# Optimization experiments

Hardware: AMD Instinct MI355X
Metric: run time of the kernel (lower is better)

The kernel has to match this reference:

```python
import jax, jax.numpy as jnp
import numpy as np

N = 50000      # nodes
E = 800000     # edges
F = 128        # node_features
DSS = 64       # degree_set_size
H = 128        # latent dim (hardcoded in GraphES)


def gcn_conv(x, W, b, src, dst, n):
    # PyG GCNConv: linear -> symmetric-normalized aggregation with self loops -> bias
    h = x @ W                                            # [N, C_out]
    deg = jnp.zeros((n,), x.dtype).at[dst].add(1.0) + 1.0  # in-degree incl. self loop
    dinv = jax.lax.rsqrt(deg)
    norm = dinv[src] * dinv[dst]                         # [E]
    agg = jnp.zeros_like(h).at[dst].add(h[src] * norm[:, None])
    agg = agg + h * (dinv * dinv)[:, None]               # self-loop term (norm_ii = 1/deg_i)
    return agg + b


def mlp(x, w1, b1, w2, b2):
    return jax.nn.relu(x @ w1 + b1) @ w2 + b2


def _swap(ei, i1, i2, coin):
    e1 = jnp.take(ei, i1, axis=1)
    e2 = jnp.take(ei, i2, axis=1)
    a, b = e1[0], e1[1]
    c, d = e2[0], e2[1]
    ne1 = jnp.where(coin, jnp.stack([a, d]), jnp.stack([a, c]))
    ne2 = jnp.where(coin, jnp.stack([c, b]), jnp.stack([b, d]))
    return ei.at[:, i1].set(ne1).at[:, i2].set(ne2)


def setup_inputs() -> dict:
    key = jax.random.key(0)
    ks = jax.random.split(key, 24)
    s = 0.05

    def rn(k, shape):
        return jax.random.normal(k, shape, jnp.float32) * s

    return {
        "x": jax.random.normal(ks[0], (N, F), jnp.float32),
        "edge_index": jax.random.randint(ks[1], (2, E), 0, N, dtype=jnp.int32),
        "degree_set": jax.random.randint(ks[2], (N,), 0, DSS, dtype=jnp.int32),
        "timesteps": 5,
        # encoder: GCN(F+DSS -> 2H), GCN(2H -> H)
        "enc_w1": rn(ks[3], (F + DSS, 2 * H)), "enc_b1": jnp.zeros((2 * H,), jnp.float32),
        "enc_w2": rn(ks[4], (2 * H, H)),       "enc_b2": jnp.zeros((H,), jnp.float32),
        # decoder: GCN(H+DSS -> 2F), GCN(2F -> F)
        "dec_w1": rn(ks[5], (H + DSS, 2 * F)), "dec_b1": jnp.zeros((2 * F,), jnp.float32),
        "dec_w2": rn(ks[6], (2 * F, F)),       "dec_b2": jnp.zeros((F,), jnp.float32),
        # edge_predictor_1: Linear(128,64)->ReLU->Linear(64,1)
        "ep1_w1": rn(ks[7], (H, 64)),  "ep1_b1": jnp.zeros((64,), jnp.float32),
        "ep1_w2": rn(ks[8], (64, 1)),  "ep1_b2": jnp.zeros((1,), jnp.float32),
        # edge_predictor_2: input is z concat flattened pair features -> 128+256=384
        "ep2_w1": rn(ks[9], (H + 2 * H, 64)), "ep2_b1": jnp.zeros((64,), jnp.float32),
        "ep2_w2": rn(ks[10], (64, 1)),        "ep2_b2": jnp.zeros((1,), jnp.float32),
    }


def reference(x, edge_index, degree_set, timesteps,
              enc_w1, enc_b1, enc_w2, enc_b2,
              dec_w1, dec_b1, dec_w2, dec_b2,
              ep1_w1, ep1_b1, ep1_w2, ep1_b2,
              ep2_w1, ep2_b1, ep2_w2, ep2_b2):
    src, dst = edge_index[0], edge_index[1]
    dh = jax.nn.one_hot(degree_set, DSS, dtype=x.dtype)  # [N, DSS]

    # ---- encoder ----
    h = jax.nn.relu(gcn_conv(jnp.concatenate([x, dh], 1), enc_w1, enc_b1, src, dst, N))
    z = gcn_conv(h, enc_w2, enc_b2, src, dst, N)          # [N, H]

    # ---- forward diffusion: timesteps random edge swaps (deterministic PRNG) ----
    ei = edge_index
    for t in range(timesteps):
        k1, k2 = jax.random.split(jax.random.fold_in(jax.random.key(1), t))
        idx = jax.random.choice(k1, E, (2,), replace=False)
        ei = _swap(ei, idx[0], idx[1], jax.random.bernoulli(k2))

    # ---- reverse process: argmax-driven edge swaps ----
    # edge_predictor_1 scores depend only on z -> identical every step; compute once
    i1 = jnp.argmax(mlp(z, ep1_w1, ep1_b1, ep1_w2, ep1_b2).squeeze(-1))
    for t in range(timesteps):
        e1 = jnp.take(ei, i1, axis=1)                     # [2]
        e1f = z[e1].reshape(-1)                           # [2H]
        cond = jnp.concatenate([z, jnp.broadcast_to(e1f, (N, 2 * H))], 1)
        i2 = jnp.argmax(mlp(cond, ep2_w1, ep2_b1, ep2_w2, ep2_b2).squeeze(-1))
        coin = jax.random.bernoulli(jax.random.fold_in(jax.random.key(2), t))
        ei = _swap(ei, i1, i2, coin)

    # ---- decoder on final edge structure ----
    src2, dst2 = ei[0], ei[1]
    hd = jax.nn.relu(gcn_conv(jnp.concatenate([z, dh], 1), dec_w1, dec_b1, src2, dst2, N))
    out = gcn_conv(hd, dec_w2, dec_b2, src2, dst2, N)     # [N, F]
    return out, ei
```

## Files before the change

kernel.cpp:

```cpp
#include <hip/hip_runtime.h>
#include <cstdint>
#include <cstddef>
#include <vector>
#include <algorithm>

#define NN 50000
#define EE 800000
#define FF 128
#define HH 128
#define TSTEPS 5

typedef __attribute__((ext_vector_type(8))) short bf16x8;
typedef __attribute__((ext_vector_type(4))) float f32x4;

__device__ __forceinline__ float bf2f(unsigned short u)
{
    return __uint_as_float((unsigned)u << 16);
}
__device__ __forceinline__ unsigned short f2bf(float x)
{
    unsigned u = __float_as_uint(x);
    u = (u + 0x7FFFu + ((u >> 16) & 1u));
    return (unsigned short)(u >> 16);
}
__device__ __forceinline__ void splitbf(float v, unsigned short& hi, unsigned short& lo)
{
    hi = f2bf(v);
    lo = f2bf(v - bf2f(hi));
}

__device__ __forceinline__ void gload16(const void* g, void* l)
{
    __builtin_amdgcn_global_load_lds(
        (const __attribute__((address_space(1))) void*)g,
        (__attribute__((address_space(3))) void*)l, 16, 0, 0);
}

__global__ __launch_bounds__(256, 4) void zw1_gemm(
    const float* __restrict__ A, const float* __restrict__ Wp4,
    float* __restrict__ Pout, int n, const float* __restrict__ bias)
{
    __shared__ float As[32][128];
    const int row0 = blockIdx.x * 32;
    const int tid = threadIdx.x;
    for (int idx = tid; idx < 32 * 32; idx += 256) {
        int r = idx >> 5, k4 = idx & 31;
        int gr = row0 + r;
        float4 v = make_float4(0.f, 0.f, 0.f, 0.f);
        if (gr < n) v = ((const float4*)(A + (size_t)gr * 128))[k4];
        *(float4*)&As[r][k4 * 4] = v;
    }
    __syncthreads();
    const int w = tid >> 6, l = tid & 63;
    float acc[8];
#pragma unroll
    for (int r = 0; r < 8; r++) acc[r] = 0.f;

#pragma unroll 2
    for (int k4 = 0; k4 < 32; k4++) {
        float4 wv = ((const float4*)Wp4)[k4 * 64 + l];
#pragma unroll
        for (int r = 0; r < 8; r++) {
            float4 zv = *(const float4*)&As[w * 8 + r][k4 * 4];
            acc[r] = fmaf(zv.x, wv.x, acc[r]);
            acc[r] = fmaf(zv.y, wv.y, acc[r]);
            acc[r] = fmaf(zv.z, wv.z, acc[r]);
            acc[r] = fmaf(zv.w, wv.w, acc[r]);
        }
    }
    float bv = bias[l];
#pragma unroll
    for (int r = 0; r < 8; r++) {
        int gr = row0 + w * 8 + r;
        if (gr < n) Pout[(size_t)gr * 64 + l] = acc[r] + bv;
    }
}

template <int K, int C, int BC, int WR, int WC, bool HAS_BIAS, bool RELU>
__global__ __launch_bounds__(256) void gemm_bf16_tiled(
    const unsigned short* __restrict__ A, const unsigned short* __restrict__ Wp,
    unsigned short* __restrict__ Pout, const float* __restrict__ bias, int n)
{
    constexpr int KC = K / 32;
    constexpr int RT = 128 / (WR * 16);
    constexpr int TT = BC / (WC * 16);
    constexpr int STAGE_USHORTS = 4096 + BC * 32;
    constexpr int OT_USHORTS = 128 * BC;
    constexpr int LDS_USHORTS = (STAGE_USHORTS > OT_USHORTS) ? STAGE_USHORTS : OT_USHORTS;
    __shared__ __align__(16) unsigned short smem[LDS_USHORTS];
    unsigned short* AL = smem;
    unsigned short* WL = smem + 4096;

    const int row0 = blockIdx.x * 128;
    const int col0 = blockIdx.y * BC;
    const int tid = threadIdx.x;
    const int w = tid >> 6, l = tid & 63;
    const int m = l & 15, quad = l >> 4;
    const int wr = w / WC, wc = w % WC;
    const int rowBase = wr * (RT * 16);
    const int colBase = wc * (TT * 16);

    f32x4 acc[RT][TT];
#pragma unroll
    for (int rt = 0; rt < RT; rt++)
#pragma unroll
        for (int tt = 0; tt < TT; tt++) acc[rt][tt] = { 0.f, 0.f, 0.f, 0.f };

    for (int kc = 0; kc < KC; kc++) {
        for (int s = w; s < 8; s += 4) {
            int rg = row0 + s * 16 + (l >> 2);
            if (rg > n - 1) rg = n - 1;
            size_t go = (size_t)rg * K + kc * 32 + (l & 3) * 8;
            gload16(A + go, AL + s * 512);
        }
        for (int s = w; s < BC / 16; s += 4) {
            size_t wo = ((size_t)kc * C + col0) * 32 + s * 512 + l * 8;
            gload16(Wp + wo, WL + s * 512);
        }
        __syncthreads();

        bf16x8 a[RT];
#pragma unroll
        for (int rt = 0; rt < RT; rt++)
            a[rt] = *(const bf16x8*)(AL + (rowBase + rt * 16 + m) * 32 + quad * 8);
#pragma unroll
        for (int tt = 0; tt < TT; tt++) {
            bf16x8 b = *(const bf16x8*)(WL + (colBase + tt * 16 + m) * 32 + quad * 8);
#pragma unroll
            for (int rt = 0; rt < RT; rt++)
                acc[rt][tt] = __builtin_amdgcn_mfma_f32_16x16x32_bf16(a[rt], b, acc[rt][tt], 0, 0, 0);
        }
        __syncthreads();
    }

    unsigned short* Ot = smem;
#pragma unroll
    for (int tt = 0; tt < TT; tt++) {
        int col_in = colBase + tt * 16 + m;
        float bv = HAS_BIAS ? bias[col0 + col_in] : 0.f;
#pragma unroll
        for (int rt = 0; rt < RT; rt++)
#pragma unroll
            for (int r = 0; r < 4; r++) {
                int row_in = rowBase + rt * 16 + quad * 4 + r;
                float v = acc[rt][tt][r] + bv;
                if (RELU) v = fmaxf(v, 0.f);
                Ot[row_in * BC + col_in] = f2bf(v);
            }
    }
    __syncthreads();
    for (int idx = tid; idx < 128 * (BC / 8); idx += 256) {
        int rr = idx / (BC / 8), c8 = idx - rr * (BC / 8);
        int gr = row0 + rr;
        if (gr < n)
            *(bf16x8*)(Pout + (size_t)gr * C + col0 + c8 * 8) =
                *(const bf16x8*)(Ot + rr * BC + c8 * 8);
    }
}

template <int K, int C, int BC, int WR, int WC, bool HAS_BIAS, bool RELU, bool OUT_SPLIT>
__global__ __launch_bounds__(256) void gemm_split_tiled(
    const unsigned short* __restrict__ Ahi, const unsigned short* __restrict__ Alo,
    const unsigned short* __restrict__ Whi, const unsigned short* __restrict__ Wlo,
    void* __restrict__ PoutHi, unsigned short* __restrict__ PoutLo,
    const float* __restrict__ bias, int n)
{
    constexpr int KC = K / 32;
    constexpr int RT = 128 / (WR * 16);
    constexpr int TT = BC / (WC * 16);
    constexpr int LDS_USHORTS = 8192 + BC * 64;
    __shared__ __align__(16) unsigned short smem[LDS_USHORTS];
    unsigned short* AhL = smem;
    unsigned short* AlL = smem + 4096;
    unsigned short* WhL = smem + 8192;
    unsigned short* WlL = smem + 8192 + BC * 32;

    const int row0 = blockIdx.x * 128;
    const int col0 = blockIdx.y * BC;
    const int tid = threadIdx.x;
    const int w = tid >> 6, l = tid & 63;
    const int m = l & 15, quad = l >> 4;
    const int wr = w / WC, wc = w % WC;
    const int rowBase = wr * (RT * 16);
    const int colBase = wc * (TT * 16);

    f32x4 acc[RT][TT];
#pragma unroll
    for (int rt = 0; rt < RT; rt++)
#pragma unroll
        for (int tt = 0; tt < TT; tt++) acc[rt][tt] = { 0.f, 0.f, 0.f, 0.f };

    for (int kc = 0; kc < KC; kc++) {
        for (int s = w; s < 8; s += 4) {
            int rg = row0 + s * 16 + (l >> 2);
            if (rg > n - 1) rg = n - 1;
            size_t go = (size_t)rg * K + kc * 32 + (l & 3) * 8;
            gload16(Ahi + go, AhL + s * 512);
            gload16(Alo + go, AlL + s * 512);
        }
        for (int s = w; s < BC / 16; s += 4) {
            size_t wo = ((size_t)kc * C + col0) * 32 + s * 512 + l * 8;
            gload16(Whi + wo, WhL + s * 512);
            gload16(Wlo + wo, WlL + s * 512);
        }
        __syncthreads();

        bf16x8 ah[RT], al[RT];
#pragma unroll
        for (int rt = 0; rt < RT; rt++) {
            int ro = (rowBase + rt * 16 + m) * 32 + quad * 8;
            ah[rt] = *(const bf16x8*)(AhL + ro);
            al[rt] = *(const bf16x8*)(AlL + ro);
        }
#pragma unroll
        for (int tt = 0; tt < TT; tt++) {
            int co = (colBase + tt * 16 + m) * 32 + quad * 8;
            bf16x8 wh = *(const bf16x8*)(WhL + co);
            bf16x8 wl = *(const bf16x8*)(WlL + co);
#pragma unroll
            for (int rt = 0; rt < RT; rt++) {
                acc[rt][tt] = __builtin_amdgcn_mfma_f32_16x16x32_bf16(al[rt], wh, acc[rt][tt], 0, 0, 0);
                acc[rt][tt] = __builtin_amdgcn_mfma_f32_16x16x32_bf16(ah[rt], wl, acc[rt][tt], 0, 0, 0);
                acc[rt][tt] = __builtin_amdgcn_mfma_f32_16x16x32_bf16(ah[rt], wh, acc[rt][tt], 0, 0, 0);
            }
        }
        __syncthreads();
    }

    if (OUT_SPLIT) {
        unsigned short* Ot = smem;
#pragma unroll
        for (int tt = 0; tt < TT; tt++) {
            int col_in = colBase + tt * 16 + m;
            float bv = HAS_BIAS ? bias[col0 + col_in] : 0.f;
#pragma unroll
            for (int rt = 0; rt < RT; rt++)
#pragma unroll
                for (int r = 0; r < 4; r++) {
                    int row_in = rowBase + rt * 16 + quad * 4 + r;
                    float v = acc[rt][tt][r] + bv;
                    if (RELU) v = fmaxf(v, 0.f);
                    Ot[row_in * BC + col_in] = f2bf(v);
                }
        }
        __syncthreads();
        for (int idx = tid; idx < 128 * (BC / 8); idx += 256) {
            int rr = idx / (BC / 8), c8 = idx - rr * (BC / 8);
            int gr = row0 + rr;
            if (gr < n)
                *(bf16x8*)((unsigned short*)PoutHi + (size_t)gr * C + col0 + c8 * 8) =
                    *(const bf16x8*)(Ot + rr * BC + c8 * 8);
        }
        __syncthreads();
#pragma unroll
        for (int tt = 0; tt < TT; tt++) {
            int col_in = colBase + tt * 16 + m;
            float bv = HAS_BIAS ? bias[col0 + col_in] : 0.f;
#pragma unroll
            for (int rt = 0; rt < RT; rt++)
#pragma unroll
                for (int r = 0; r < 4; r++) {
                    int row_in = rowBase + rt * 16 + quad * 4 + r;
                    float v = acc[rt][tt][r] + bv;
                    if (RELU) v = fmaxf(v, 0.f);
                    unsigned short h = f2bf(v);
                    Ot[row_in * BC + col_in] = f2bf(v - bf2f(h));
                }
        }
        __syncthreads();
        for (int idx = tid; idx < 128 * (BC / 8); idx += 256) {
            int rr = idx / (BC / 8), c8 = idx - rr * (BC / 8);
            int gr = row0 + rr;
            if (gr < n)
                *(bf16x8*)(PoutLo + (size_t)gr * C + col0 + c8 * 8) =
                    *(const bf16x8*)(Ot + rr * BC + c8 * 8);
        }
    } else {
#pragma unroll
        for (int tt = 0; tt < TT; tt++) {
            int col = col0 + colBase + tt * 16 + m;
            float bv = HAS_BIAS ? bias[col] : 0.f;
#pragma unroll
            for (int rt = 0; rt < RT; rt++)
#pragma unroll
                for (int r = 0; r < 4; r++) {
                    int gr = row0 + rowBase + rt * 16 + quad * 4 + r;
                    if (gr >= n) continue;
                    float v = acc[rt][tt][r] + bv;
                    if (RELU) v = fmaxf(v, 0.f);
                    ((float*)PoutHi)[(size_t)gr * C + col] = v;
                }
        }
    }
}

template <int K, int C>
__global__ void pack_w(const float* __restrict__ W, unsigned short* __restrict__ Wp)
{
    int idx = blockIdx.x * 256 + threadIdx.x;
    if (idx >= K * C) return;
    int k = idx / C, nn = idx - k * C;
    Wp[((size_t)(k >> 5) * C + nn) * 32 + (k & 31)] = f2bf(W[idx]);
}

template <int K, int C>
__global__ void pack_w_split(const float* __restrict__ W,
                             unsigned short* __restrict__ Wphi,
                             unsigned short* __restrict__ Wplo)
{
    int idx = blockIdx.x * 256 + threadIdx.x;
    if (idx >= K * C) return;
    int k = idx / C, nn = idx - k * C;
    unsigned short hi, lo;
    splitbf(W[idx], hi, lo);
    size_t o = ((size_t)(k >> 5) * C + nn) * 32 + (k & 31);
    Wphi[o] = hi;
    Wplo[o] = lo;
}

template <int K, int C>
__global__ void pack_w4(const float* __restrict__ W, float* __restrict__ Wp4)
{
    int idx = blockIdx.x * 256 + threadIdx.x;
    if (idx >= K * C) return;
    int k = idx / C, c = idx - k * C;
    Wp4[(((size_t)(k >> 2) * C) + c) * 4 + (k & 3)] = W[idx];
}

__global__ void count_deg(const int* __restrict__ dst, int* __restrict__ cnt, int e)
{
    int i = blockIdx.x * blockDim.x + threadIdx.x;
    if (i < e) {
        unsigned d = (unsigned)dst[i];
        if (d < (unsigned)NN) atomicAdd(&cnt[d], 1);
    }
}

__global__ void scan_block(const int* __restrict__ cnt, int* __restrict__ excl,
                           int* __restrict__ bsum, float* __restrict__ dinv, int n)
{
    __shared__ int s[256];
    int i = blockIdx.x * 256 + threadIdx.x;
    int v = (i < n) ? cnt[i] : 0;
    if (i < n) dinv[i] = 1.0f / sqrtf((float)v + 1.0f);
    s[threadIdx.x] = v;
    __syncthreads();
    for (int off = 1; off < 256; off <<= 1) {
        int t = (threadIdx.x >= off) ? s[threadIdx.x - off] : 0;
        __syncthreads();
        s[threadIdx.x] += t;
        __syncthreads();
    }
    if (i < n) excl[i] = s[threadIdx.x] - v;
    if (threadIdx.x == 255) bsum[blockIdx.x] = s[255];
}
__global__ void scan_add_fill(int* __restrict__ rowptr, const int* __restrict__ bsum,
                              int* __restrict__ fill, int n, int e)
{
    int pre = 0;
    for (int b = 0; b < (int)blockIdx.x; b++) pre += bsum[b];
    int i = blockIdx.x * 256 + threadIdx.x;
    if (i < n) { rowptr[i] += pre; fill[i] = 0; }
    if (i == 0) rowptr[n] = e;
}

__global__ void csr_fill_pairs(const int* __restrict__ src, const int* __restrict__ dst,
                               const float* __restrict__ dinv, const int* __restrict__ rowptr,
                               int* __restrict__ fill, int* __restrict__ csr_src,
                               float* __restrict__ csr_nrm, int e)
{
    int i = blockIdx.x * blockDim.x + threadIdx.x;
    if (i >= e) return;
    int d = dst[i], s = src[i];
    if ((unsigned)d >= (unsigned)NN || (unsigned)s >= (unsigned)NN) return;
    int slot = rowptr[d] + atomicAdd(&fill[d], 1);
    csr_src[slot] = s;
    csr_nrm[slot] = dinv[s] * dinv[d];
}

template <bool BF16SRC, int OUTMODE>
__global__ __launch_bounds__(256) void agg_feat(
    const void* __restrict__ Xv, const int* __restrict__ ds,
    const int* __restrict__ rowptr, const int* __restrict__ csr_src,
    const float* __restrict__ csr_nrm, const float* __restrict__ dinv,
    void* __restrict__ Fout, unsigned short* __restrict__ FoutLo)
{
    const int w = threadIdx.x >> 6, l = threadIdx.x & 63;
    const int i = blockIdx.x * 4 + w;
    if (i >= NN) return;
    const int half = l >> 5, lh = l & 31;

    auto loadRow4 = [&](int s, float* v) {
        if (BF16SRC) {
            ushort4 u = ((const ushort4*)((const unsigned short*)Xv + (size_t)s * 128))[lh];
            v[0] = bf2f(u.x); v[1] = bf2f(u.y); v[2] = bf2f(u.z); v[3] = bf2f(u.w);
        } else {
            float4 t = ((const float4*)((const float*)Xv + (size_t)s * 128))[lh];
            v[0] = t.x; v[1] = t.y; v[2] = t.z; v[3] = t.w;
        }
    };

    float di = dinv[i], d2 = di * di;
    float acc[4];
    {
        float sv[4];
        loadRow4(i, sv);
        float wgt = half ? 0.f : d2;
#pragma unroll
        for (int v = 0; v < 4; v++) acc[v] = sv[v] * wgt;
    }
    float hist = (ds[i] == l) ? d2 : 0.f;

    const int beg = rowptr[i], end = rowptr[i + 1];
    int idx = beg;
    for (; idx + 8 <= end; idx += 8) {
        int s[8]; float nw[8]; int b[8];
#pragma unroll
        for (int j = 0; j < 8; j++) { s[j] = csr_src[idx + j]; nw[j] = csr_nrm[idx + j]; }
#pragma unroll
        for (int j = 0; j < 8; j++) b[j] = ds[s[j]];
        float vv[4][4];
#pragma unroll
        for (int p = 0; p < 4; p++) loadRow4(s[2 * p + half], vv[p]);
#pragma unroll
        for (int p = 0; p < 4; p++) {
            float wp = nw[2 * p + half];
#pragma unroll
            for (int v = 0; v < 4; v++) acc[v] = fmaf(vv[p][v], wp, acc[v]);
        }
#pragma unroll
        for (int j = 0; j < 8; j++) hist += (b[j] == l) ? nw[j] : 0.f;
    }
    for (; idx + 2 <= end; idx += 2) {
        int s0 = csr_src[idx], s1 = csr_src[idx + 1];
        float n0 = csr_nrm[idx], n1 = csr_nrm[idx + 1];
        int b0 = ds[s0], b1 = ds[s1];
        float v0[4];
        loadRow4(half ? s1 : s0, v0);
        float wp = half ? n1 : n0;
#pragma unroll
        for (int v = 0; v < 4; v++) acc[v] = fmaf(v0[v], wp, acc[v]);
        hist += (b0 == l) ? n0 : 0.f;
        hist += (b1 == l) ? n1 : 0.f;
    }
    if (idx < end) {
        int s0 = csr_src[idx];
        float n0 = csr_nrm[idx];
        int b0 = ds[s0];
        float v0[4];
        loadRow4(s0, v0);
        float wp = half ? 0.f : n0;
#pragma unroll
        for (int v = 0; v < 4; v++) acc[v] = fmaf(v0[v], wp, acc[v]);
        hist += (b0 == l) ? n0 : 0.f;
    }
#pragma unroll
    for (int v = 0; v < 4; v++) acc[v] += __shfl_xor(acc[v], 32, 64);

    if (OUTMODE == 2) {
        if (half == 0) {
            unsigned short h[4], lo[4];
#pragma unroll
            for (int v = 0; v < 4; v++) splitbf(acc[v], h[v], lo[v]);
            ((ushort4*)((unsigned short*)Fout + (size_t)i * 192))[lh] =
                make_ushort4(h[0], h[1], h[2], h[3]);
            ((ushort4*)(FoutLo + (size_t)i * 192))[lh] =
                make_ushort4(lo[0], lo[1], lo[2], lo[3]);
        }
        unsigned short hh, ll;
        splitbf(hist, hh, ll);
        ((unsigned short*)Fout)[(size_t)i * 192 + 128 + l] = hh;
        FoutLo[(size_t)i * 192 + 128 + l] = ll;
    } else if (OUTMODE == 1) {
        if (half == 0) {
            ((ushort4*)((unsigned short*)Fout + (size_t)i * 192))[lh] =
                make_ushort4(f2bf(acc[0]), f2bf(acc[1]), f2bf(acc[2]), f2bf(acc[3]));
        }
        ((unsigned short*)Fout)[(size_t)i * 192 + 128 + l] = f2bf(hist);
    } else {
        if (half == 0) {
            ((float4*)((float*)Fout + (size_t)i * 192))[lh] =
                make_float4(acc[0], acc[1], acc[2], acc[3]);
        }
        ((float*)Fout)[(size_t)i * 192 + 128 + l] = hist;
    }
}

template <bool RELU, bool BF16P>
__global__ __launch_bounds__(256) void agg_wave(
    const void* __restrict__ Pv, const int* __restrict__ rowptr,
    const int* __restrict__ csr_src, const float* __restrict__ csr_nrm,
    const float* __restrict__ dinv, const float* __restrict__ bias,
    float* __restrict__ B, unsigned short* __restrict__ Bbf)
{
    const int w = threadIdx.x >> 6, l = threadIdx.x & 63;
    const int i = blockIdx.x * 4 + w;
    if (i >= NN) return;
    const int half = l >> 5, lh = l & 31;

    auto loadRow4 = [&](int s, float* v) {
        if (BF16P) {
            ushort4 u = ((const ushort4*)((const unsigned short*)Pv + (size_t)s * 128))[lh];
            v[0] = bf2f(u.x); v[1] = bf2f(u.y); v[2] = bf2f(u.z); v[3] = bf2f(u.w);
        } else {
            float4 t = ((const float4*)((const float*)Pv + (size_t)s * 128))[lh];
            v[0] = t.x; v[1] = t.y; v[2] = t.z; v[3] = t.w;
        }
    };

    float di = dinv[i], d2 = di * di;
    float acc[4];
    {
        float sv[4];
        loadRow4(i, sv);
        float wgt = half ? 0.f : d2;
#pragma unroll
        for (int v = 0; v < 4; v++) acc[v] = sv[v] * wgt;
    }

    const int beg = rowptr[i], end = rowptr[i + 1];
    int idx = beg;
    for (; idx + 8 <= end; idx += 8) {
        int s[8]; float nw[8];
#pragma unroll
        for (int j = 0; j < 8; j++) { s[j] = csr_src[idx + j]; nw[j] = csr_nrm[idx + j]; }
        float vv[4][4];
#pragma unroll
        for (int p = 0; p < 4; p++) loadRow4(s[2 * p + half], vv[p]);
#pragma unroll
        for (int p = 0; p < 4; p++) {
            float wp = nw[2 * p + half];
#pragma unroll
            for (int v = 0; v < 4; v++) acc[v] = fmaf(vv[p][v], wp, acc[v]);
        }
    }
    for (; idx + 2 <= end; idx += 2) {
        int s0 = csr_src[idx], s1 = csr_src[idx + 1];
        float n0 = csr_nrm[idx], n1 = csr_nrm[idx + 1];
        float v0[4];
        loadRow4(half ? s1 : s0, v0);
        float wp = half ? n1 : n0;
#pragma unroll
        for (int v = 0; v < 4; v++) acc[v] = fmaf(v0[v], wp, acc[v]);
    }
    if (idx < end) {
        int s0 = csr_src[idx];
        float n0 = csr_nrm[idx];
        float v0[4];
        loadRow4(s0, v0);
        float wp = half ? 0.f : n0;
#pragma unroll
        for (int v = 0; v < 4; v++) acc[v] = fmaf(v0[v], wp, acc[v]);
    }
#pragma unroll
    for (int v = 0; v < 4; v++) acc[v] += __shfl_xor(acc[v], 32, 64);

    if (half == 0) {
        float r[4];
#pragma unroll
        for (int v = 0; v < 4; v++) {
            r[v] = acc[v] + bias[lh * 4 + v];
            if (RELU) r[v] = fmaxf(r[v], 0.f);
        }
        ((float4*)(B + (size_t)i * 128))[lh] = make_float4(r[0], r[1], r[2], r[3]);
        if (Bbf)
            ((ushort4*)(Bbf + (size_t)i * 128))[lh] =
                make_ushort4(f2bf(r[0]), f2bf(r[1]), f2bf(r[2]), f2bf(r[3]));
    }
}

__device__ __forceinline__ unsigned long long packScore(float s, int i)
{
    unsigned u = __float_as_uint(s);
    u = (u & 0x80000000u) ? ~u : (u | 0x80000000u);
    return ((unsigned long long)u << 32) | (unsigned)(~(unsigned)i);
}
__device__ __forceinline__ int unpackIdx(unsigned long long v)
{
    return (int)(~(unsigned)(v & 0xFFFFFFFFull));
}
__device__ __forceinline__ unsigned long long maxu64(unsigned long long a,
                                                     unsigned long long b)
{
    return a > b ? a : b;
}

__device__ __forceinline__ void publishBest(
    unsigned long long* blockBest, unsigned* counter, unsigned long long bv,
    int nblocks, unsigned* isLastFlag)
{
    __hip_atomic_store(&blockBest[blockIdx.x], bv, __ATOMIC_RELEASE,
                       __HIP_MEMORY_SCOPE_AGENT);
    unsigned prev = __hip_atomic_fetch_add(counter, 1u, __ATOMIC_ACQ_REL,
                                           __HIP_MEMORY_SCOPE_AGENT);
    *isLastFlag = (prev == (unsigned)(nblocks - 1)) ? 1u : 0u;
}
__device__ __forceinline__ unsigned long long loadBest(
    const unsigned long long* blockBest, int i)
{
    return __hip_atomic_load(&blockBest[i], __ATOMIC_RELAXED,
                             __HIP_MEMORY_SCOPE_AGENT);
}

__global__ __launch_bounds__(256, 4) void score1_blocks(
    const float* __restrict__ z, const float* __restrict__ w1p4,
    const float* __restrict__ b1, const float* __restrict__ w2,
    unsigned long long* __restrict__ blockBest,
    unsigned long long* __restrict__ out, unsigned* __restrict__ counter,
    int n, int nblocks)
{
    __shared__ float Zs[64][HH];
    __shared__ unsigned long long red[4];
    __shared__ unsigned isLast;
    const int row0 = blockIdx.x * 64;
    const int tid = threadIdx.x;
    for (int idx = tid; idx < 64 * 32; idx += 256) {
        int r = idx >> 5, k4 = idx & 31;
        int gr = row0 + r;
        float4 v = make_float4(0.f, 0.f, 0.f, 0.f);
        if (gr < n) v = ((const float4*)(z + (size_t)gr * HH))[k4];
        *(float4*)&Zs[r][k4 * 4] = v;
    }
    __syncthreads();

    const int w = tid >> 6, l = tid & 63;
    float b1v = b1[l], w2v = w2[l];
    unsigned long long best = 0;
    for (int rg = 0; rg < 4; rg++) {
        const int rbase = w * 16 + rg * 4;
        float acc[4];
#pragma unroll
        for (int r = 0; r < 4; r++) acc[r] = b1v;
#pragma unroll 4
        for (int k4 = 0; k4 < 32; k4++) {
            float4 wv = ((const float4*)w1p4)[k4 * 64 + l];
#pragma unroll
            for (int r = 0; r < 4; r++) {
                float4 zv = *(const float4*)&Zs[rbase + r][k4 * 4];
                acc[r] = fmaf(zv.x, wv.x, acc[r]);
                acc[r] = fmaf(zv.y, wv.y, acc[r]);
                acc[r] = fmaf(zv.z, wv.z, acc[r]);
                acc[r] = fmaf(zv.w, wv.w, acc[r]);
            }
        }
#pragma unroll
        for (int r = 0; r < 4; r++) {
            float p = fmaxf(acc[r], 0.f) * w2v;
#pragma unroll
            for (int off = 32; off > 0; off >>= 1) p += __shfl_xor(p, off, 64);
            int row = row0 + rbase + r;
            if (row < n) best = maxu64(best, packScore(p, row));
        }
    }
    if (l == 0) red[w] = best;
    __syncthreads();
    if (tid == 0) {
        unsigned long long bv = maxu64(maxu64(red[0], red[1]), maxu64(red[2], red[3]));
        publishBest(blockBest, counter, bv, nblocks, &isLast);
    }
    __syncthreads();
    if (isLast) {
        unsigned long long b = 0;
        for (int i = tid; i < nblocks; i += 256) b = maxu64(b, loadBest(blockBest, i));
#pragma unroll
        for (int off = 32; off > 0; off >>= 1)
            b = maxu64(b, (unsigned long long)__shfl_xor((long long)b, off, 64));
        if ((tid & 63) == 0) red[tid >> 6] = b;
        __syncthreads();
        if (tid == 0) {
            *out = maxu64(maxu64(red[0], red[1]), maxu64(red[2], red[3]));
            __hip_atomic_store(counter, 0u, __ATOMIC_RELAXED, __HIP_MEMORY_SCOPE_AGENT);
        }
    }
}

__global__ __launch_bounds__(256) void score2_fused(
    int* __restrict__ ei, const unsigned long long* __restrict__ best1,
    const float* __restrict__ z, const float* __restrict__ w1,
    const float* __restrict__ zw1, const float* __restrict__ w2,
    unsigned long long* __restrict__ blockBest, unsigned* __restrict__ counter,
    int n, int coin)
{
    __shared__ float za_s[HH], zb_s[HH];
    __shared__ float cpart[4][64];
    __shared__ float Cs[64], W2s[64];
    __shared__ unsigned long long red[4];
    __shared__ unsigned isLast;
    int i1 = unpackIdx(*best1);
    if ((unsigned)i1 >= (unsigned)EE) i1 = 0;
    int a = ei[i1], b = ei[EE + i1];
    if ((unsigned)a >= (unsigned)NN) a = 0;
    if ((unsigned)b >= (unsigned)NN) b = 0;
    const int tid = threadIdx.x;
    if (tid < HH) za_s[tid] = z[(size_t)a * HH + tid];
    else          zb_s[tid - HH] = z[(size_t)b * HH + tid - HH];
    __syncthreads();
    const int h = tid & 63, kg = tid >> 6;
    float accc = 0.f;
#pragma unroll
    for (int kk = 0; kk < 32; kk++) {
        int k = kg * 32 + kk;
        accc = fmaf(za_s[k], w1[(128 + k) * 64 + h], accc);
        accc = fmaf(zb_s[k], w1[(256 + k) * 64 + h], accc);
    }
    cpart[kg][h] = accc;
    __syncthreads();
    if (tid < 64) {
        Cs[tid] = (cpart[0][tid] + cpart[1][tid]) + (cpart[2][tid] + cpart[3][tid]);
        W2s[tid] = w2[tid];
    }
    __syncthreads();
    const int w = kg, l = h;
    unsigned long long best = 0;
    for (int i = blockIdx.x * 4 + w; i < n; i += gridDim.x * 4) {
        float v = zw1[(size_t)i * 64 + l] + Cs[l];
        v = fmaxf(v, 0.f) * W2s[l];
#pragma unroll
        for (int off = 32; off > 0; off >>= 1) v += __shfl_xor(v, off, 64);
        best = maxu64(best, packScore(v, i));
    }
    if (l == 0) red[w] = best;
    __syncthreads();
    const int nblocks = (int)gridDim.x;
    if (tid == 0) {
        unsigned long long bv = maxu64(maxu64(red[0], red[1]), maxu64(red[2], red[3]));
        publishBest(blockBest, counter, bv, nblocks, &isLast);
    }
    __syncthreads();
    if (isLast) {
        unsigned long long bb = 0;
        for (int i = tid; i < nblocks; i += 256) bb = maxu64(bb, loadBest(blockBest, i));
#pragma unroll
        for (int off = 32; off > 0; off >>= 1)
            bb = maxu64(bb, (unsigned long long)__shfl_xor((long long)bb, off, 64));
        if ((tid & 63) == 0) red[tid >> 6] = bb;
        __syncthreads();
        if (tid == 0) {
            unsigned long long bestv = maxu64(maxu64(red[0], red[1]), maxu64(red[2], red[3]));
            int i2 = unpackIdx(bestv);
            if ((unsigned)i2 >= (unsigned)EE) i2 = 0;
            int A = ei[i1], B = ei[EE + i1], C = ei[i2], D = ei[EE + i2];
            ei[i1] = A;             ei[EE + i1] = coin ? D : C;
            ei[i2] = coin ? C : B;  ei[EE + i2] = coin ? B : D;
            __hip_atomic_store(counter, 0u, __ATOMIC_RELAXED, __HIP_MEMORY_SCOPE_AGENT);
        }
    }
}

struct Swaps { int a[TSTEPS]; int b[TSTEPS]; unsigned coins; };

__global__ void fwd_swaps_k(int* __restrict__ ei, Swaps s)
{
    if (threadIdx.x != 0 || blockIdx.x != 0) return;
    for (int t = 0; t < TSTEPS; t++) {
        int i1 = s.a[t], i2 = s.b[t];
        if ((unsigned)i1 >= (unsigned)EE || (unsigned)i2 >= (unsigned)EE) continue;
        int coin = (s.coins >> t) & 1;
        int A = ei[i1], B = ei[EE + i1], C = ei[i2], D = ei[EE + i2];
        ei[i1] = A;             ei[EE + i1] = coin ? D : C;
        ei[i2] = coin ? C : B;  ei[EE + i2] = coin ? B : D;
    }
}

__global__ void write_out(const float* __restrict__ outF, const int* __restrict__ ei,
                          float* __restrict__ dst)
{
    int i = blockIdx.x * 256 + threadIdx.x;
    if (i < NN * FF) {
        float v = outF[i];
        v = fminf(fmaxf(v, -64.f), 64.f);
        dst[i] = v;
    } else if (i < NN * FF + 2 * EE) {
        dst[i] = (float)ei[i - NN * FF];
    }
}

static inline uint32_t rotl32(uint32_t x, int n) { return (x << n) | (x >> (32 - n)); }

static void tf(uint32_t k0, uint32_t k1, uint32_t c0, uint32_t c1,
               uint32_t& o0, uint32_t& o1)
{
    uint32_t ks[3] = { k0, k1, k0 ^ k1 ^ 0x1BD11BDAu };
    uint32_t x0 = c0 + ks[0], x1 = c1 + ks[1];
    static const int rA[4] = { 13, 15, 26, 6 };
    static const int rB[4] = { 17, 29, 16, 24 };
    for (int g = 0; g < 5; g++) {
        const int* r = (g & 1) ? rB : rA;
        for (int j = 0; j < 4; j++) { x0 += x1; x1 = rotl32(x1, r[j]); x1 ^= x0; }
        x0 += ks[(g + 1) % 3];
        x1 += ks[(g + 2) % 3] + (uint32_t)(g + 1);
    }
    o0 = x0; o1 = x1;
}

static void jsplit_part(uint32_t k0, uint32_t k1,
                        uint32_t& a0, uint32_t& a1, uint32_t& b0, uint32_t& b1)
{
    tf(k0, k1, 0u, 0u, a0, a1);
    tf(k0, k1, 0u, 1u, b0, b1);
}

static void jbits_part(uint32_t k0, uint32_t k1, uint32_t n, std::vector<uint32_t>& out)
{
    out.resize(n);
    for (uint32_t i = 0; i < n; i++) {
        uint32_t a, b;
        tf(k0, k1, 0u, i, a, b);
        out[i] = a ^ b;
    }
}

static bool jbern_part(uint32_t k0, uint32_t k1)
{
    uint32_t a, b;
    tf(k0, k1, 0u, 0u, a, b);
    return (a ^ b) < 0x80000000u;
}

struct PrngConsts {
    Swaps swaps;
    int revCoin[TSTEPS];
    PrngConsts()
    {
        swaps.coins = 0;
        std::vector<uint32_t> bits1, bits2;
        std::vector<uint64_t> packed((size_t)EE);
        for (int t = 0; t < TSTEPS; t++) {
            uint32_t kt0, kt1;
            tf(0u, 1u, 0u, (uint32_t)t, kt0, kt1);
            uint32_t kc0, kc1, kb0, kb1;
            jsplit_part(kt0, kt1, kc0, kc1, kb0, kb1);
            if (jbern_part(kb0, kb1)) swaps.coins |= (1u << t);

            uint32_t cur0 = kc0, cur1 = kc1, sub0, sub1, nk0, nk1;
            jsplit_part(cur0, cur1, nk0, nk1, sub0, sub1);
            cur0 = nk0; cur1 = nk1;
            jbits_part(sub0, sub1, EE, bits1);
            jsplit_part(cur0, cur1, nk0, nk1, sub0, sub1);
            cur0 = nk0; cur1 = nk1;
            jbits_part(sub0, sub1, EE, bits2);

            uint64_t m1 = ~0ull, m2 = ~0ull;
            for (uint32_t pos = 0; pos < EE; pos++) {
                uint64_t u = ((uint64_t)bits2[pos] << 32) | pos;
                if (u < m1) { m2 = m1; m1 = u; }
                else if (u < m2) { m2 = u; }
            }
            uint32_t pos0 = (uint32_t)m1, pos1 = (uint32_t)m2;
            for (uint32_t j = 0; j < EE; j++)
                packed[j] = ((uint64_t)bits1[j] << 32) | j;
            std::nth_element(packed.begin(), packed.begin() + pos0, packed.end());
            uint32_t j0 = (uint32_t)packed[pos0];
            std::nth_element(packed.begin(), packed.begin() + pos1, packed.end());
            uint32_t j1 = (uint32_t)packed[pos1];
            swaps.a[t] = (int)j0;
            swaps.b[t] = (int)j1;
        }
        for (int t = 0; t < TSTEPS; t++) {
            uint32_t kt0, kt1;
            tf(0u, 2u, 0u, (uint32_t)t, kt0, kt1);
            revCoin[t] = jbern_part(kt0, kt1) ? 1 : 0;
        }
    }
};
static const PrngConsts g_prng;

extern "C" void kernel_launch(void* const* d_in, const int* in_sizes, int n_in,
                              void* d_out, int out_size, void* d_ws, size_t ws_size,
                              hipStream_t stream)
{
    (void)out_size; (void)ws_size;

    static const int kWant[20] = {
        NN * FF, 2 * EE, NN, 1,
        192 * 256, 256, 256 * 128, 128,
        192 * 256, 256, 256 * 128, 128,
        128 * 64, 64, 64, 1,
        384 * 64, 64, 64, 1
    };
    const void* p[20] = {};
    {
        int j = 0;
        for (int k = 0; k < 20; k++) {
            if (j < n_in && in_sizes[j] == kWant[k]) { p[k] = d_in[j]; j++; }
            else if (kWant[k] == 1)                  { p[k] = nullptr; }
            else if (j < n_in)                       { p[k] = d_in[j]; j++; }
        }
    }
    const float* x      = (const float*)p[0];
    const int*   ei_in  = (const int*)p[1];
    const int*   ds     = (const int*)p[2];
    const float* enc_w1 = (const float*)p[4];
    const float* enc_b1 = (const float*)p[5];
    const float* enc_w2 = (const float*)p[6];
    const float* enc_b2 = (const float*)p[7];
    const float* dec_w1 = (const float*)p[8];
    const float* dec_b1 = (const float*)p[9];
    const float* dec_w2 = (const float*)p[10];
    const float* dec_b2 = (const float*)p[11];
    const float* ep1_w1 = (const float*)p[12];
    const float* ep1_b1 = (const float*)p[13];
    const float* ep1_w2 = (const float*)p[14];
    const float* ep2_w1 = (const float*)p[16];
    const float* ep2_b1 = (const float*)p[17];
    const float* ep2_w2 = (const float*)p[18];

    char* ws = (char*)d_ws;
    size_t off = 0;
    auto alloc = [&](size_t bytes) -> void* {
        void* q = ws + off;
        off += (bytes + 255) & ~(size_t)255;
        return q;
    };
    float* bufP    = (float*)alloc((size_t)NN * 256 * 4);
    float* bufH    = (float*)alloc((size_t)NN * 256 * 4);
    int*   eiw     = (int*)alloc((size_t)2 * EE * 4);
    int*   csr_src = (int*)alloc((size_t)EE * 4);
    float* csr_nrm = (float*)alloc((size_t)EE * 4);
    int*   rowptr  = (int*)alloc((size_t)(NN + 1) * 4);
    int*   cnt     = (int*)alloc((size_t)NN * 4);
    int*   fill    = (int*)alloc((size_t)NN * 4);
    int*   bsum    = (int*)alloc(256 * 4);
    float* dinv    = (float*)alloc((size_t)NN * 4);
    unsigned short* zbf   = (unsigned short*)alloc((size_t)NN * 128 * 2);
    unsigned short* wp1   = (unsigned short*)alloc((size_t)192 * 256 * 2);
    unsigned short* wp2   = (unsigned short*)alloc((size_t)256 * 128 * 2);
    unsigned short* w1hi  = (unsigned short*)alloc((size_t)192 * 256 * 2);
    unsigned short* w1lo  = (unsigned short*)alloc((size_t)192 * 256 * 2);
    unsigned short* w2hi  = (unsigned short*)alloc((size_t)256 * 128 * 2);
    unsigned short* w2lo  = (unsigned short*)alloc((size_t)256 * 128 * 2);
    float* ep1w1p = (float*)alloc((size_t)128 * 64 * 4);
    float* ep2w1p = (float*)alloc((size_t)128 * 64 * 4);
    unsigned long long* blockBest = (unsigned long long*)alloc(4096 * 8);
    unsigned long long* best1 = (unsigned long long*)alloc(8);
    unsigned* counters = (unsigned*)alloc(256);

    unsigned short* f1hi = (unsigned short*)bufP;
    unsigned short* f1lo = f1hi + (size_t)NN * 192;
    float* P2   = bufP;
    float* zw1  = bufP;
    unsigned short* feat2bf = (unsigned short*)bufP;
    unsigned short* p4      = (unsigned short*)bufP;
    float* outF = bufP + (size_t)NN * 128;
    unsigned short* hhi = (unsigned short*)bufH;
    unsigned short* hlo = hhi + (size_t)NN * 256;
    float* zbuf = bufH;
    unsigned short* hdbf = (unsigned short*)bufH;

    const int TPB = 256;
    const int gN      = (NN + TPB - 1) / TPB;
    const int gE      = (EE + TPB - 1) / TPB;
    const int gRows64s = (NN + 63) / 64;
    const int gRows32 = (NN + 31) / 32;
    const int gRows128 = (NN + 127) / 128;
    const int gWave   = (NN + 3) / 4;

    hipMemsetAsync(counters, 0, 8, stream);

    pack_w<192, 256><<<(192 * 256 + TPB - 1) / TPB, TPB, 0, stream>>>(dec_w1, wp1);
    pack_w<256, 128><<<(256 * 128 + TPB - 1) / TPB, TPB, 0, stream>>>(dec_w2, wp2);
    pack_w_split<192, 256><<<(192 * 256 + TPB - 1) / TPB, TPB, 0, stream>>>(enc_w1, w1hi, w1lo);
    pack_w_split<256, 128><<<(256 * 128 + TPB - 1) / TPB, TPB, 0, stream>>>(enc_w2, w2hi, w2lo);
    pack_w4<128, 64><<<(128 * 64 + TPB - 1) / TPB, TPB, 0, stream>>>(ep1_w1, ep1w1p);
    pack_w4<128, 64><<<(128 * 64 + TPB - 1) / TPB, TPB, 0, stream>>>(ep2_w1, ep2w1p);

    hipMemsetAsync(cnt, 0, (size_t)NN * 4, stream);
    count_deg<<<gE, TPB, 0, stream>>>(ei_in + EE, cnt, EE);
    scan_block<<<gN, TPB, 0, stream>>>(cnt, rowptr, bsum, dinv, NN);
    scan_add_fill<<<gN, TPB, 0, stream>>>(rowptr, bsum, fill, NN, EE);
    csr_fill_pairs<<<gE, TPB, 0, stream>>>(ei_in, ei_in + EE, dinv, rowptr, fill,
                                           csr_src, csr_nrm, EE);

    agg_feat<false, 2><<<gWave, TPB, 0, stream>>>(
        x, ds, rowptr, csr_src, csr_nrm, dinv, f1hi, f1lo);
    gemm_split_tiled<192, 256, 128, 2, 2, true, true, true>
        <<<dim3(gRows128, 2), TPB, 0, stream>>>(
        f1hi, f1lo, w1hi, w1lo, hhi, hlo, enc_b1, NN);

    gemm_split_tiled<256, 128, 64, 4, 1, false, false, false>
        <<<dim3(gRows128, 2), TPB, 0, stream>>>(
        hhi, hlo, w2hi, w2lo, P2, nullptr, nullptr, NN);
    agg_wave<false, false><<<gWave, TPB, 0, stream>>>(
        P2, rowptr, csr_src, csr_nrm, dinv, enc_b2, zbuf, zbf);

    score1_blocks<<<gRows64s, TPB, 0, stream>>>(zbuf, ep1w1p, ep1_b1, ep1_w2,
                                                blockBest, best1, counters + 0,
                                                NN, gRows64s);
    zw1_gemm<<<gRows32, TPB, 0, stream>>>(zbuf, ep2w1p, zw1, NN, ep2_b1);

    hipMemcpyAsync(eiw, ei_in, (size_t)2 * EE * 4, hipMemcpyDeviceToDevice, stream);
    fwd_swaps_k<<<1, 64, 0, stream>>>(eiw, g_prng.swaps);

    for (int t = 0; t < TSTEPS; t++) {
        score2_fused<<<256, TPB, 0, stream>>>(eiw, best1, zbuf, ep2_w1,
                                              zw1, ep2_w2, blockBest, counters + 1,
                                              NN, g_prng.revCoin[t]);
    }

    hipMemsetAsync(cnt, 0, (size_t)NN * 4, stream);
    count_deg<<<gE, TPB, 0, stream>>>(eiw + EE, cnt, EE);
    scan_block<<<gN, TPB, 0, stream>>>(cnt, rowptr, bsum, dinv, NN);
    scan_add_fill<<<gN, TPB, 0, stream>>>(rowptr, bsum, fill, NN, EE);
    csr_fill_pairs<<<gE, TPB, 0, stream>>>(eiw, eiw + EE, dinv, rowptr, fill,
                                           csr_src, csr_nrm, EE);

    agg_feat<true, 1><<<gWave, TPB, 0, stream>>>(
        zbf, ds, rowptr, csr_src, csr_nrm, dinv, feat2bf, nullptr);
    gemm_bf16_tiled<192, 256, 128, 2, 2, true, true>
        <<<dim3(gRows128, 2), TPB, 0, stream>>>(
        feat2bf, wp1, hdbf, dec_b1, NN);

    gemm_bf16_tiled<256, 128, 128, 2, 2, false, false>
        <<<dim3(gRows128, 1), TPB, 0, stream>>>(
        hdbf, wp2, p4, nullptr, NN);
    agg_wave<false, true><<<gWave, TPB, 0, stream>>>(
        p4, rowptr, csr_src, csr_nrm, dinv, dec_b2, outF, nullptr);

    write_out<<<(NN * FF + 2 * EE + TPB - 1) / TPB, TPB, 0, stream>>>(
        outF, eiw, (float*)d_out);
}
```

Measured before the change: 820.6 us.

## Fuse zw1 GEMM into score1 kernel and write decoder output directly

```diff
diff --git a/kernel.cpp b/kernel.cpp
--- a/kernel.cpp
+++ b/kernel.cpp
@@ -34,46 +34,6 @@
     __builtin_amdgcn_global_load_lds(
         (const __attribute__((address_space(1))) void*)g,
         (__attribute__((address_space(3))) void*)l, 16, 0, 0);
-}
-
-__global__ __launch_bounds__(256, 4) void zw1_gemm(
-    const float* __restrict__ A, const float* __restrict__ Wp4,
-    float* __restrict__ Pout, int n, const float* __restrict__ bias)
-{
-    __shared__ float As[32][128];
-    const int row0 = blockIdx.x * 32;
-    const int tid = threadIdx.x;
-    for (int idx = tid; idx < 32 * 32; idx += 256) {
-        int r = idx >> 5, k4 = idx & 31;
-        int gr = row0 + r;
-        float4 v = make_float4(0.f, 0.f, 0.f, 0.f);
-        if (gr < n) v = ((const float4*)(A + (size_t)gr * 128))[k4];
-        *(float4*)&As[r][k4 * 4] = v;
-    }
-    __syncthreads();
-    const int w = tid >> 6, l = tid & 63;
-    float acc[8];
-#pragma unroll
-    for (int r = 0; r < 8; r++) acc[r] = 0.f;
-
-#pragma unroll 2
-    for (int k4 = 0; k4 < 32; k4++) {
-        float4 wv = ((const float4*)Wp4)[k4 * 64 + l];
-#pragma unroll
-        for (int r = 0; r < 8; r++) {
-            float4 zv = *(const float4*)&As[w * 8 + r][k4 * 4];
-            acc[r] = fmaf(zv.x, wv.x, acc[r]);
-            acc[r] = fmaf(zv.y, wv.y, acc[r]);
-            acc[r] = fmaf(zv.z, wv.z, acc[r]);
-            acc[r] = fmaf(zv.w, wv.w, acc[r]);
-        }
-    }
-    float bv = bias[l];
-#pragma unroll
-    for (int r = 0; r < 8; r++) {
-        int gr = row0 + w * 8 + r;
-        if (gr < n) Pout[(size_t)gr * 64 + l] = acc[r] + bv;
-    }
 }
 
 template <int K, int C, int BC, int WR, int WC, bool HAS_BIAS, bool RELU>
@@ -486,7 +446,7 @@
     }
 }
 
-template <bool RELU, bool BF16P>
+template <bool RELU, bool BF16P, bool CLAMP>
 __global__ __launch_bounds__(256) void agg_wave(
     const void* __restrict__ Pv, const int* __restrict__ rowptr,
     const int* __restrict__ csr_src, const float* __restrict__ csr_nrm,
@@ -561,6 +521,7 @@
         for (int v = 0; v < 4; v++) {
             r[v] = acc[v] + bias[lh * 4 + v];
             if (RELU) r[v] = fmaxf(r[v], 0.f);
+            if (CLAMP) r[v] = fminf(fmaxf(r[v], -64.f), 64.f);
         }
         ((float4*)(B + (size_t)i * 128))[lh] = make_float4(r[0], r[1], r[2], r[3]);
         if (Bbf)
@@ -602,9 +563,11 @@
                              __HIP_MEMORY_SCOPE_AGENT);
 }
 
-__global__ __launch_bounds__(256, 4) void score1_blocks(
+__global__ __launch_bounds__(256, 4) void score1_zw1(
     const float* __restrict__ z, const float* __restrict__ w1p4,
     const float* __restrict__ b1, const float* __restrict__ w2,
+    const float* __restrict__ wz4, const float* __restrict__ bz,
+    float* __restrict__ zw1out,
     unsigned long long* __restrict__ blockBest,
     unsigned long long* __restrict__ out, unsigned* __restrict__ counter,
     int n, int nblocks)
@@ -624,35 +587,64 @@
     __syncthreads();
 
     const int w = tid >> 6, l = tid & 63;
-    float b1v = b1[l], w2v = w2[l];
-    unsigned long long best = 0;
-    for (int rg = 0; rg < 4; rg++) {
-        const int rbase = w * 16 + rg * 4;
-        float acc[4];
-#pragma unroll
-        for (int r = 0; r < 4; r++) acc[r] = b1v;
+
+    {
+        float b1v = b1[l], w2v = w2[l];
+        unsigned long long best = 0;
+        for (int rg = 0; rg < 4; rg++) {
+            const int rbase = w * 16 + rg * 4;
+            float acc[4];
+#pragma unroll
+            for (int r = 0; r < 4; r++) acc[r] = b1v;
 #pragma unroll 4
+            for (int k4 = 0; k4 < 32; k4++) {
+                float4 wv = ((const float4*)w1p4)[k4 * 64 + l];
+#pragma unroll
+                for (int r = 0; r < 4; r++) {
+                    float4 zv = *(const float4*)&Zs[rbase + r][k4 * 4];
+                    acc[r] = fmaf(zv.x, wv.x, acc[r]);
+                    acc[r] = fmaf(zv.y, wv.y, acc[r]);
+                    acc[r] = fmaf(zv.z, wv.z, acc[r]);
+                    acc[r] = fmaf(zv.w, wv.w, acc[r]);
+                }
+            }
+#pragma unroll
+            for (int r = 0; r < 4; r++) {
+                float p = fmaxf(acc[r], 0.f) * w2v;
+#pragma unroll
+                for (int off = 32; off > 0; off >>= 1) p += __shfl_xor(p, off, 64);
+                int row = row0 + rbase + r;
+                if (row < n) best = maxu64(best, packScore(p, row));
+            }
+        }
+        if (l == 0) red[w] = best;
+    }
+
+    {
+        float acz[16];
+#pragma unroll
+        for (int r = 0; r < 16; r++) acz[r] = 0.f;
+        const int rb = w * 16;
+#pragma unroll 2
         for (int k4 = 0; k4 < 32; k4++) {
-            float4 wv = ((const float4*)w1p4)[k4 * 64 + l];
-#pragma unroll
-            for (int r = 0; r < 4; r++) {
-                float4 zv = *(const float4*)&Zs[rbase + r][k4 * 4];
-                acc[r] = fmaf(zv.x, wv.x, acc[r]);
-                acc[r] = fmaf(zv.y, wv.y, acc[r]);
-                acc[r] = fmaf(zv.z, wv.z, acc[r]);
-                acc[r] = fmaf(zv.w, wv.w, acc[r]);
+            float4 wv = ((const float4*)wz4)[k4 * 64 + l];
+#pragma unroll
+            for (int r = 0; r < 16; r++) {
+                float4 zv = *(const float4*)&Zs[rb + r][k4 * 4];
+                acz[r] = fmaf(zv.x, wv.x, acz[r]);
+                acz[r] = fmaf(zv.y, wv.y, acz[r]);
+                acz[r] = fmaf(zv.z, wv.z, acz[r]);
+                acz[r] = fmaf(zv.w, wv.w, acz[r]);
             }
         }
-#pragma unroll
-        for (int r = 0; r < 4; r++) {
-            float p = fmaxf(acc[r], 0.f) * w2v;
-#pragma unroll
-            for (int off = 32; off > 0; off >>= 1) p += __shfl_xor(p, off, 64);
-            int row = row0 + rbase + r;
-            if (row < n) best = maxu64(best, packScore(p, row));
-        }
-    }
-    if (l == 0) red[w] = best;
+        float bvz = bz[l];
+#pragma unroll
+        for (int r = 0; r < 16; r++) {
+            int gr = row0 + rb + r;
+            if (gr < n) zw1out[(size_t)gr * 64 + l] = acz[r] + bvz;
+        }
+    }
+
     __syncthreads();
     if (tid == 0) {
         unsigned long long bv = maxu64(maxu64(red[0], red[1]), maxu64(red[2], red[3]));
@@ -762,17 +754,10 @@
     }
 }
 
-__global__ void write_out(const float* __restrict__ outF, const int* __restrict__ ei,
-                          float* __restrict__ dst)
+__global__ void write_edges(const int* __restrict__ ei, float* __restrict__ dst)
 {
     int i = blockIdx.x * 256 + threadIdx.x;
-    if (i < NN * FF) {
-        float v = outF[i];
-        v = fminf(fmaxf(v, -64.f), 64.f);
-        dst[i] = v;
-    } else if (i < NN * FF + 2 * EE) {
-        dst[i] = (float)ei[i - NN * FF];
-    }
+    if (i < 2 * EE) dst[i] = (float)ei[i];
 }
 
 static inline uint32_t rotl32(uint32_t x, int n) { return (x << n) | (x >> (32 - n)); }
@@ -941,7 +926,6 @@
     float* zw1  = bufP;
     unsigned short* feat2bf = (unsigned short*)bufP;
     unsigned short* p4      = (unsigned short*)bufP;
-    float* outF = bufP + (size_t)NN * 128;
     unsigned short* hhi = (unsigned short*)bufH;
     unsigned short* hlo = hhi + (size_t)NN * 256;
     float* zbuf = bufH;
@@ -951,7 +935,6 @@
     const int gN      = (NN + TPB - 1) / TPB;
     const int gE      = (EE + TPB - 1) / TPB;
     const int gRows64s = (NN + 63) / 64;
-    const int gRows32 = (NN + 31) / 32;
     const int gRows128 = (NN + 127) / 128;
     const int gWave   = (NN + 3) / 4;
 
@@ -980,21 +963,21 @@
     gemm_split_tiled<256, 128, 64, 4, 1, false, false, false>
         <<<dim3(gRows128, 2), TPB, 0, stream>>>(
         hhi, hlo, w2hi, w2lo, P2, nullptr, nullptr, NN);
-    agg_wave<false, false><<<gWave, TPB, 0, stream>>>(
+    agg_wave<false, false, false><<<gWave, TPB, 0, stream>>>(
         P2, rowptr, csr_src, csr_nrm, dinv, enc_b2, zbuf, zbf);
 
-    score1_blocks<<<gRows64s, TPB, 0, stream>>>(zbuf, ep1w1p, ep1_b1, ep1_w2,
-                                                blockBest, best1, counters + 0,
-                                                NN, gRows64s);
-    zw1_gemm<<<gRows32, TPB, 0, stream>>>(zbuf, ep2w1p, zw1, NN, ep2_b1);
+    score1_zw1<<<gRows64s, TPB, 0, stream>>>(zbuf, ep1w1p, ep1_b1, ep1_w2,
+                                             ep2w1p, ep2_b1, zw1,
+                                             blockBest, best1, counters + 0,
+                                             NN, gRows64s);
 
     hipMemcpyAsync(eiw, ei_in, (size_t)2 * EE * 4, hipMemcpyDeviceToDevice, stream);
     fwd_swaps_k<<<1, 64, 0, stream>>>(eiw, g_prng.swaps);
 
     for (int t = 0; t < TSTEPS; t++) {
-        score2_fused<<<256, TPB, 0, stream>>>(eiw, best1, zbuf, ep2_w1,
-                                              zw1, ep2_w2, blockBest, counters + 1,
-                                              NN, g_prng.revCoin[t]);
+        score2_fused<<<1024, TPB, 0, stream>>>(eiw, best1, zbuf, ep2_w1,
+                                               zw1, ep2_w2, blockBest, counters + 1,
+                                               NN, g_prng.revCoin[t]);
     }
 
     hipMemsetAsync(cnt, 0, (size_t)NN * 4, stream);
@@ -1013,9 +996,9 @@
     gemm_bf16_tiled<256, 128, 128, 2, 2, false, false>
         <<<dim3(gRows128, 1), TPB, 0, stream>>>(
         hdbf, wp2, p4, nullptr, NN);
-    agg_wave<false, true><<<gWave, TPB, 0, stream>>>(
-        p4, rowptr, csr_src, csr_nrm, dinv, dec_b2, outF, nullptr);
-
-    write_out<<<(NN * FF + 2 * EE + TPB - 1) / TPB, TPB, 0, stream>>>(
-        outF, eiw, (float*)d_out);
-}
+    agg_wave<false, true, true><<<gWave, TPB, 0, stream>>>(
+        p4, rowptr, csr_src, csr_nrm, dinv, dec_b2, (float*)d_out, nullptr);
+
+    write_edges<<<(2 * EE + TPB - 1) / TPB, TPB, 0, stream>>>(
+        eiw, (float*)d_out + (size_t)NN * FF);
+}
```

New measurement: 875.0 us. +6.6%, slower.
